# Kernel optimization log

Hardware: AMD Instinct MI355X
Metric: run time of the kernel (lower is better)

Reference implementation:

```python
import jax, jax.numpy as jnp
import numpy as np

B, V, N, IN_F, HEADS, OUT_F = 4, 4, 1000, 64, 4, 32
D = HEADS * OUT_F  # 128, concat=True
E = 64000
NEG_SLOPE = 0.2


def setup_inputs() -> dict:
    key = jax.random.key(0)
    ks = jax.random.split(key, 8)
    x = jax.random.normal(ks[0], (B, V, N, IN_F), jnp.float32)
    edge_index = jax.random.randint(ks[1], (2, E), 0, B * N, dtype=jnp.int64)
    W = jax.random.normal(ks[2], (HEADS * OUT_F, IN_F), jnp.float32) / np.sqrt(IN_F)
    att = jax.random.normal(ks[3], (1, HEADS, 2 * OUT_F), jnp.float32) * 0.1
    in_proj_w = jax.random.normal(ks[4], (3 * D, D), jnp.float32) / np.sqrt(D)
    in_proj_b = jnp.zeros((3 * D,), jnp.float32)
    out_proj_w = jax.random.normal(ks[5], (D, D), jnp.float32) / np.sqrt(D)
    out_proj_b = jnp.zeros((D,), jnp.float32)
    bias = jnp.zeros((D,), jnp.float32)
    return dict(x=x, W=W, att=att, in_proj_w=in_proj_w, in_proj_b=in_proj_b,
                out_proj_w=out_proj_w, out_proj_b=out_proj_b, bias=bias,
                edge_index=edge_index)


def reference(x, W, att, in_proj_w, in_proj_b, out_proj_w, out_proj_b, bias, edge_index):
    Bx, Vx, Nx, _ = x.shape
    Ntot = Bx * Nx
    # intra-view GAT: shared W across views
    h = jnp.einsum('bvni,oi->bvno', x, W).reshape(Bx, Vx, Nx, HEADS, OUT_F)
    # block-diagonal placement: h_full[b*V+v, b*N:(b+1)*N] = h[b,v]
    ib = jnp.arange(Bx)
    hf = jnp.zeros((Bx, Vx, Bx, Nx, HEADS, OUT_F), x.dtype).at[ib, :, ib].set(h)
    h_full = hf.reshape(Bx * Vx, Ntot, HEADS, OUT_F)
    # add self loops
    loops = jnp.arange(Ntot, dtype=edge_index.dtype)
    src = jnp.concatenate([edge_index[0], loops])
    dst = jnp.concatenate([edge_index[1], loops])
    # attention scores (faithful to source: flatten h_full over (B*V, Ntot) and
    # index with raw node ids, i.e. gathers from block 0 only)
    h_flat = h_full.reshape(Bx * Vx * Ntot, HEADS, OUT_F)
    h_cat = jnp.concatenate([h_flat[src], h_flat[dst]], axis=-1)  # [Etot, H, 2*OUT]
    att_in = jax.nn.leaky_relu(h_cat, NEG_SLOPE)
    scores = jnp.sum(att * att_in, axis=-1)  # [Etot, HEADS]
    # per-destination segment softmax
    seg_max = jax.ops.segment_max(scores, dst, num_segments=Ntot)
    seg_max = jax.lax.stop_gradient(jnp.where(jnp.isfinite(seg_max), seg_max, 0.0))
    ex = jnp.exp(scores - seg_max[dst])
    denom = jax.ops.segment_sum(ex, dst, num_segments=Ntot)
    alpha = ex / (denom[dst] + 1e-16)  # [Etot, HEADS]
    # scatter-add aggregation, broadcast over B*V rows
    msgs = h_full[:, src] * alpha[None, :, :, None]  # [B*V, Etot, H, OUT]
    out_full = jnp.zeros_like(h_full).at[:, dst].add(msgs)
    # extract each graph's own node block
    out = out_full.reshape(Bx, Vx, Bx, Nx, HEADS, OUT_F)[ib, :, ib]  # [B,V,N,H,OUT]
    h_gat = out.reshape(Bx, Vx, Nx, HEADS * OUT_F)  # concat heads
    # inter-view mixing: MHA over the V axis per node
    seq = h_gat.transpose(0, 2, 1, 3).reshape(Bx * Nx, Vx, D)
    q, k, v = jnp.split(seq @ in_proj_w.T + in_proj_b, 3, axis=-1)
    hd = D // HEADS
    sp = lambda t: t.reshape(Bx * Nx, Vx, HEADS, hd).transpose(0, 2, 1, 3)
    q, k, v = sp(q), sp(k), sp(v)
    aw = jax.nn.softmax(jnp.einsum('bhqd,bhkd->bhqk', q, k) / jnp.sqrt(jnp.asarray(hd, x.dtype)), axis=-1)
    ao = jnp.einsum('bhqk,bhkd->bhqd', aw, v).transpose(0, 2, 1, 3).reshape(Bx * Nx, Vx, D)
    mixed = ao @ out_proj_w.T + out_proj_b
    h_mixed = mixed.reshape(Bx, Nx, Vx, D).transpose(0, 2, 1, 3)  # [B,V,N,D]
    return h_mixed + bias
```

## Files before the change

kernel.cpp:

```cpp
#include <hip/hip_runtime.h>

#define NN 1000
#define HEADS_ 4
#define DM 128
#define EE 64000
#define NTOT 4000
#define ETOT 68000
#define CAP 48
#define EB 34

template <int K, int SCORE>
__device__ void gemm_tile(int mi, int ni,
                          const float* __restrict__ A, const float* __restrict__ Wt,
                          float* __restrict__ C, int N,
                          const float* __restrict__ att,
                          float* __restrict__ ssrc, float* __restrict__ sdst) {
  __shared__ float As[128 * 64];
  __shared__ float Bs[64 * 64];
  int tid = threadIdx.x;
  int m0 = mi * 128, n0 = ni * 64;
  int tx = tid & 15, ty = tid >> 4;
  const float4* A4 = (const float4*)A;
  const float4* W4 = (const float4*)Wt;
  float acc[8][4] = {};

  for (int c = 0; c < K / 64; ++c) {
    __syncthreads();
    {
      int q = tid & 15;
      int r0 = tid >> 4;
#pragma unroll
      for (int p = 0; p < 8; ++p) {
        int r = r0 + p * 16;
        float4 v = A4[(size_t)(m0 + r) * (K / 4) + c * 16 + q];
        *(float4*)&As[r * 64 + ((q ^ ((r >> 2) & 15)) << 2)] = v;
      }
#pragma unroll
      for (int p = 0; p < 4; ++p) {
        int r = r0 + p * 16;
        float4 v = W4[(size_t)(n0 + r) * (K / 4) + c * 16 + q];
        *(float4*)&Bs[r * 64 + ((q ^ ((r >> 2) & 15)) << 2)] = v;
      }
    }
    __syncthreads();
#pragma unroll 4
    for (int q = 0; q < 16; ++q) {
      float4 a[8], b[4];
#pragma unroll
      for (int i = 0; i < 8; ++i) {
        int r = ty * 8 + i;
        a[i] = *(const float4*)&As[r * 64 + ((q ^ ((r >> 2) & 15)) << 2)];
      }
#pragma unroll
      for (int j = 0; j < 4; ++j) {
        int rn = tx * 4 + j;
        b[j] = *(const float4*)&Bs[rn * 64 + ((q ^ ((rn >> 2) & 15)) << 2)];
      }
#pragma unroll
      for (int i = 0; i < 8; ++i)
#pragma unroll
        for (int j = 0; j < 4; ++j)
          acc[i][j] += a[i].x * b[j].x + a[i].y * b[j].y
                     + a[i].z * b[j].z + a[i].w * b[j].w;
    }
  }

  int nc = n0 + tx * 4;
#pragma unroll
  for (int i = 0; i < 8; ++i) {
    int m = m0 + ty * 8 + i;
    float4 o = make_float4(acc[i][0], acc[i][1], acc[i][2], acc[i][3]);
    *(float4*)&C[(size_t)m * N + nc] = o;
  }

  if (SCORE && m0 < NN) {
    int hsel = tx >> 3;
    int h = ni * 2 + hsel;
    int kb = (tx & 7) * 4;
    float a0[4], a1[4];
#pragma unroll
    for (int j = 0; j < 4; ++j) {
      a0[j] = att[h * 64 + kb + j];
      a1[j] = att[h * 64 + 32 + kb + j];
    }
#pragma unroll
    for (int i = 0; i < 8; ++i) {
      int m = m0 + ty * 8 + i;
      float p0 = 0.f, p1 = 0.f;
#pragma unroll
      for (int j = 0; j < 4; ++j) {
        float g = acc[i][j];
        float lr = g > 0.f ? g : 0.2f * g;
        p0 += a0[j] * lr;
        p1 += a1[j] * lr;
      }
      p0 += __shfl_xor(p0, 1, 16); p1 += __shfl_xor(p1, 1, 16);
      p0 += __shfl_xor(p0, 2, 16); p1 += __shfl_xor(p1, 2, 16);
      p0 += __shfl_xor(p0, 4, 16); p1 += __shfl_xor(p1, 4, 16);
      if ((tx & 7) == 0 && m < NN) {
        ssrc[m * HEADS_ + h] = p0;
        sdst[m * HEADS_ + h] = p1;
      }
    }
  }
}

__global__ __launch_bounds__(256) void k1_kernel(const float* __restrict__ x,
                                                 const float* __restrict__ W,
                                                 const float* __restrict__ att,
                                                 float* __restrict__ hbuf,
                                                 float* __restrict__ ssrc,
                                                 float* __restrict__ sdst,
                                                 const int* __restrict__ ei,
                                                 int* __restrict__ cnt,
                                                 int* __restrict__ elist) {
  int bid = blockIdx.x;
  if (bid < 250) {
    gemm_tile<64, 1>(bid >> 1, bid & 1, x, W, hbuf, 128, att, ssrc, sdst);
  } else {
    for (int e = (bid - 250) * 256 + threadIdx.x; e < ETOT; e += EB * 256) {
      int s, d;
      if (e < EE) { s = ei[e]; d = ei[EE + e]; }
      else { s = d = e - EE; }
      int pos = atomicAdd(&cnt[d], 1);
      if (pos < CAP) elist[d * CAP + pos] = s;
    }
  }
}

__global__ __launch_bounds__(256) void gather_kernel(const int* __restrict__ cnt,
                                                     const int* __restrict__ elist,
                                                     const float* __restrict__ ssrc,
                                                     const float* __restrict__ sdst,
                                                     const float* __restrict__ hbuf,
                                                     float* __restrict__ hgat) {
  __shared__ int   srcs[2][CAP];
  __shared__ float exs[2][CAP][HEADS_];
  int li = threadIdx.x >> 7;
  int t = threadIdx.x & 127;
  int d = blockIdx.x * 2 + li;
  int b = d / NN;
  int v = t >> 5, q = t & 31, h = q >> 3;
  int m = cnt[d]; if (m > CAP) m = CAP;
  for (int base = 0; base < m; base += 32) {
    int i = base + (t >> 2);
    if (i < m) {
      int s = elist[d * CAP + i];
      if ((t & 3) == 0) srcs[li][i] = s;
      float sc = ssrc[s * HEADS_ + (t & 3)] + sdst[d * HEADS_ + (t & 3)];
      exs[li][i][t & 3] = __expf(sc);
    }
  }
  __syncthreads();
  float den = 1e-16f;
  float4 acc = make_float4(0.f, 0.f, 0.f, 0.f);
  const float* hbase = hbuf + ((size_t)(b * 4 + v) * NN) * DM + q * 4;
  for (int i = 0; i < m; ++i) {
    float ex = exs[li][i][h];
    den += ex;
    unsigned sl = (unsigned)(srcs[li][i] - b * NN);
    if (sl < NN) {
      float4 hv = *(const float4*)(hbase + (size_t)sl * DM);
      acc.x += ex * hv.x; acc.y += ex * hv.y;
      acc.z += ex * hv.z; acc.w += ex * hv.w;
    }
  }
  float r = 1.f / den;
  acc.x *= r; acc.y *= r; acc.z *= r; acc.w *= r;
  *(float4*)&hgat[((size_t)(d * 4 + v)) * DM + q * 4] = acc;
}

#define QS 388

__global__ __launch_bounds__(512) void fused3_kernel(const float* __restrict__ hgat,
                                                     const float* __restrict__ inw,
                                                     const float* __restrict__ inb,
                                                     const float* __restrict__ outw,
                                                     const float* __restrict__ outb,
                                                     const float* __restrict__ bias,
                                                     float* __restrict__ out) {
  extern __shared__ float smem[];
  float* As = smem;
  float* Bs = smem + 4096;
  float* qk = smem + 12288;
  float* ao = qk;

  int tid = threadIdx.x;
  int g0 = blockIdx.x * 16;
  int tx = tid & 31, ty = tid >> 5;

  const float4* H4 = (const float4*)(hgat + (size_t)(g0 * 4) * DM);
  const float4* W4 = (const float4*)inw;

  float acc[3][4][4] = {};
#pragma unroll
  for (int c = 0; c < 2; ++c) {
#pragma unroll
    for (int ni = 0; ni < 3; ++ni) {
      __syncthreads();
      {
        int q = tid & 15, r0 = tid >> 4;
        if (ni == 0) {
#pragma unroll
          for (int p = 0; p < 2; ++p) {
            int r = r0 + p * 32;
            float4 v = H4[r * 32 + c * 16 + q];
            *(float4*)&As[r * 64 + ((q ^ ((r >> 2) & 15)) << 2)] = v;
          }
        }
#pragma unroll
        for (int p = 0; p < 4; ++p) {
          int r = r0 + p * 32;
          float4 v = W4[(size_t)(ni * 128 + r) * 32 + c * 16 + q];
          *(float4*)&Bs[r * 64 + ((q ^ ((r >> 2) & 15)) << 2)] = v;
        }
      }
      __syncthreads();
#pragma unroll 4
      for (int q = 0; q < 16; ++q) {
        float4 a[4], b[4];
        int sa = (q ^ ty) << 2;
        int sb = (q ^ (tx & 15)) << 2;
#pragma unroll
        for (int i = 0; i < 4; ++i)
          a[i] = *(const float4*)&As[(ty * 4 + i) * 64 + sa];
#pragma unroll
        for (int j = 0; j < 4; ++j)
          b[j] = *(const float4*)&Bs[(tx * 4 + j) * 64 + sb];
#pragma unroll
        for (int i = 0; i < 4; ++i)
#pragma unroll
          for (int j = 0; j < 4; ++j)
            acc[ni][i][j] += a[i].x * b[j].x + a[i].y * b[j].y
                           + a[i].z * b[j].z + a[i].w * b[j].w;
      }
    }
  }

#pragma unroll
  for (int ni = 0; ni < 3; ++ni) {
    int nc = ni * 128 + tx * 4;
    float4 bb = *(const float4*)&inb[nc];
#pragma unroll
    for (int i = 0; i < 4; ++i) {
      int r = ty * 4 + i;
      *(float4*)&qk[r * QS + nc] =
          make_float4(acc[ni][i][0] + bb.x, acc[ni][i][1] + bb.y,
                      acc[ni][i][2] + bb.z, acc[ni][i][3] + bb.w);
    }
  }
  __syncthreads();

  int ln = tid >> 5;
  int vq2 = (tid >> 3) & 3, h2 = (tid >> 1) & 3, s2 = tid & 1;
  float aww[4];
  {
    const float* qr = &qk[(ln * 4 + vq2) * QS + h2 * 32 + s2 * 16];
    float4 qv[4];
#pragma unroll
    for (int u = 0; u < 4; ++u) qv[u] = *(const float4*)&qr[u * 4];
    float sc[4];
#pragma unroll
    for (int vk = 0; vk < 4; ++vk) {
      const float* kr = &qk[(ln * 4 + vk) * QS + 128 + h2 * 32 + s2 * 16];
      float s = 0.f;
#pragma unroll
      for (int u = 0; u < 4; ++u) {
        float4 kv = *(const float4*)&kr[u * 4];
        s += qv[u].x * kv.x + qv[u].y * kv.y + qv[u].z * kv.z + qv[u].w * kv.w;
      }
      sc[vk] = s;
    }
#pragma unroll
    for (int vk = 0; vk < 4; ++vk)
      sc[vk] = (sc[vk] + __shfl_xor(sc[vk], 1)) * 0.17677669529663687f;
    float mx = fmaxf(fmaxf(sc[0], sc[1]), fmaxf(sc[2], sc[3]));
    float e0 = __expf(sc[0] - mx), e1 = __expf(sc[1] - mx);
    float e2 = __expf(sc[2] - mx), e3 = __expf(sc[3] - mx);
    float inv = 1.f / (e0 + e1 + e2 + e3);
    aww[0] = e0 * inv; aww[1] = e1 * inv; aww[2] = e2 * inv; aww[3] = e3 * inv;
  }

  float4 o[4];
#pragma unroll
  for (int u = 0; u < 4; ++u) o[u] = make_float4(0.f, 0.f, 0.f, 0.f);
#pragma unroll
  for (int vk = 0; vk < 4; ++vk) {
    const float* vr = &qk[(ln * 4 + vk) * QS + 256 + h2 * 32 + s2 * 16];
    float w = aww[vk];
#pragma unroll
    for (int u = 0; u < 4; ++u) {
      float4 vv = *(const float4*)&vr[u * 4];
      o[u].x += w * vv.x; o[u].y += w * vv.y;
      o[u].z += w * vv.z; o[u].w += w * vv.w;
    }
  }
  __syncthreads();
  {
    int r = ln * 4 + vq2;
#pragma unroll
    for (int u = 0; u < 4; ++u) {
      int qp = h2 * 8 + s2 * 4 + u;
      int cc = qp >> 4, qg = qp & 15;
      *(float4*)&ao[cc * 4096 + r * 64 + ((qg ^ (ln & 15)) << 2)] = o[u];
    }
  }
  __syncthreads();

  float oc[4][4] = {};
  const float4* O4 = (const float4*)outw;
#pragma unroll
  for (int c = 0; c < 2; ++c) {
    {
      int q = tid & 15, r0 = tid >> 4;
#pragma unroll
      for (int p = 0; p < 4; ++p) {
        int r = r0 + p * 32;
        float4 v = O4[(size_t)r * 32 + c * 16 + q];
        *(float4*)&Bs[r * 64 + ((q ^ ((r >> 2) & 15)) << 2)] = v;
      }
    }
    __syncthreads();
#pragma unroll 4
    for (int q = 0; q < 16; ++q) {
      float4 a[4], b[4];
      int sa = (q ^ ty) << 2;
      int sb = (q ^ (tx & 15)) << 2;
#pragma unroll
      for (int i = 0; i < 4; ++i)
        a[i] = *(const float4*)&ao[c * 4096 + (ty * 4 + i) * 64 + sa];
#pragma unroll
      for (int j = 0; j < 4; ++j)
        b[j] = *(const float4*)&Bs[(tx * 4 + j) * 64 + sb];
#pragma unroll
      for (int i = 0; i < 4; ++i)
#pragma unroll
        for (int j = 0; j < 4; ++j)
          oc[i][j] += a[i].x * b[j].x + a[i].y * b[j].y
                    + a[i].z * b[j].z + a[i].w * b[j].w;
    }
    __syncthreads();
  }

  {
    int nc = tx * 4;
    float4 ob = make_float4(outb[nc] + bias[nc], outb[nc + 1] + bias[nc + 1],
                            outb[nc + 2] + bias[nc + 2], outb[nc + 3] + bias[nc + 3]);
#pragma unroll
    for (int i = 0; i < 4; ++i) {
      int r = ty * 4 + i;
      int node = g0 + (r >> 2), v = r & 3;
      int bg = node / NN, n = node - bg * NN;
      int om = (bg * 4 + v) * NN + n;
      *(float4*)&out[(size_t)om * DM + nc] =
          make_float4(oc[i][0] + ob.x, oc[i][1] + ob.y,
                      oc[i][2] + ob.z, oc[i][3] + ob.w);
    }
  }
}

extern "C" void kernel_launch(void* const* d_in, const int* in_sizes, int n_in,
                              void* d_out, int out_size, void* d_ws, size_t ws_size,
                              hipStream_t stream) {
  const float* x    = (const float*)d_in[0];
  const float* W    = (const float*)d_in[1];
  const float* att  = (const float*)d_in[2];
  const float* inw  = (const float*)d_in[3];
  const float* inb  = (const float*)d_in[4];
  const float* outw = (const float*)d_in[5];
  const float* outb = (const float*)d_in[6];
  const float* bias = (const float*)d_in[7];
  const int*   ei   = (const int*)d_in[8];
  float* out = (float*)d_out;

  float* ws = (float*)d_ws;
  float* hbuf  = ws;
  float* hgat  = ws + 2100000;
  float* ssrc  = ws + 12500000;
  float* sdst  = ssrc + 16000;
  int*   cnt   = (int*)(sdst + 16000);
  int*   elist = cnt + 4000;

  static int lds_opt_in = 0;
  if (!lds_opt_in) {
    hipFuncSetAttribute((const void*)fused3_kernel,
                        hipFuncAttributeMaxDynamicSharedMemorySize, 160 * 1024);
    lds_opt_in = 1;
  }

  hipMemsetAsync(ssrc, 0, 36000 * sizeof(float), stream);

  k1_kernel<<<250 + EB, 256, 0, stream>>>(x, W, att, hbuf, ssrc, sdst, ei, cnt, elist);
  gather_kernel<<<NTOT / 2, 256, 0, stream>>>(cnt, elist, ssrc, sdst, hbuf, hgat);
  fused3_kernel<<<250, 512, 148480, stream>>>(hgat, inw, inb, outw, outb, bias, out);
}
```

Measured before the change: 144.4 us.

## Fuse GAT gather into MHA kernel and shrink first GEMM tile

The neighbour gather/softmax-aggregation stage is folded into the inter-view attention kernel. Each block now builds its 64 rows of aggregated features directly in shared memory instead of writing hgat to global memory and reading it back, which also removes one kernel launch. The first projection GEMM switches from 128x64 to 64x64 tiles, doubling its block count to 500 for better occupancy. The trade-off is that the gather now runs with only 250 blocks and a different thread mapping, giving it less parallelism for latency hiding.

```diff
diff --git a/kernel.cpp b/kernel.cpp
--- a/kernel.cpp
+++ b/kernel.cpp
@@ -8,56 +8,54 @@
 #define ETOT 68000
 #define CAP 48
 #define EB 34
-
-template <int K, int SCORE>
-__device__ void gemm_tile(int mi, int ni,
-                          const float* __restrict__ A, const float* __restrict__ Wt,
-                          float* __restrict__ C, int N,
-                          const float* __restrict__ att,
-                          float* __restrict__ ssrc, float* __restrict__ sdst) {
-  __shared__ float As[128 * 64];
+#define QS 388
+
+template <int KK, int SCORE>
+__device__ void gemm64(int mi, int ni,
+                       const float* __restrict__ A, const float* __restrict__ Wt,
+                       float* __restrict__ C, int N,
+                       const float* __restrict__ att,
+                       float* __restrict__ ssrc, float* __restrict__ sdst) {
+  __shared__ float As[64 * 64];
   __shared__ float Bs[64 * 64];
   int tid = threadIdx.x;
-  int m0 = mi * 128, n0 = ni * 64;
+  int m0 = mi * 64, n0 = ni * 64;
   int tx = tid & 15, ty = tid >> 4;
   const float4* A4 = (const float4*)A;
   const float4* W4 = (const float4*)Wt;
-  float acc[8][4] = {};
-
-  for (int c = 0; c < K / 64; ++c) {
+  float acc[4][4] = {};
+
+  for (int c = 0; c < KK / 64; ++c) {
     __syncthreads();
     {
-      int q = tid & 15;
-      int r0 = tid >> 4;
-#pragma unroll
-      for (int p = 0; p < 8; ++p) {
-        int r = r0 + p * 16;
-        float4 v = A4[(size_t)(m0 + r) * (K / 4) + c * 16 + q];
-        *(float4*)&As[r * 64 + ((q ^ ((r >> 2) & 15)) << 2)] = v;
-      }
+      int q = tid & 15, r0 = tid >> 4;
 #pragma unroll
       for (int p = 0; p < 4; ++p) {
         int r = r0 + p * 16;
-        float4 v = W4[(size_t)(n0 + r) * (K / 4) + c * 16 + q];
+        float4 v = A4[(size_t)(m0 + r) * (KK / 4) + c * 16 + q];
+        *(float4*)&As[r * 64 + ((q ^ ((r >> 2) & 15)) << 2)] = v;
+      }
+#pragma unroll
+      for (int p = 0; p < 4; ++p) {
+        int r = r0 + p * 16;
+        float4 v = W4[(size_t)(n0 + r) * (KK / 4) + c * 16 + q];
         *(float4*)&Bs[r * 64 + ((q ^ ((r >> 2) & 15)) << 2)] = v;
       }
     }
     __syncthreads();
 #pragma unroll 4
     for (int q = 0; q < 16; ++q) {
-      float4 a[8], b[4];
-#pragma unroll
-      for (int i = 0; i < 8; ++i) {
-        int r = ty * 8 + i;
-        a[i] = *(const float4*)&As[r * 64 + ((q ^ ((r >> 2) & 15)) << 2)];
-      }
-#pragma unroll
-      for (int j = 0; j < 4; ++j) {
-        int rn = tx * 4 + j;
-        b[j] = *(const float4*)&Bs[rn * 64 + ((q ^ ((rn >> 2) & 15)) << 2)];
-      }
-#pragma unroll
-      for (int i = 0; i < 8; ++i)
+      float4 a[4], b[4];
+      int sa = (q ^ ty) << 2;
+      int sb = (q ^ tx) << 2;
+#pragma unroll
+      for (int i = 0; i < 4; ++i)
+        a[i] = *(const float4*)&As[(ty * 4 + i) * 64 + sa];
+#pragma unroll
+      for (int j = 0; j < 4; ++j)
+        b[j] = *(const float4*)&Bs[(tx * 4 + j) * 64 + sb];
+#pragma unroll
+      for (int i = 0; i < 4; ++i)
 #pragma unroll
         for (int j = 0; j < 4; ++j)
           acc[i][j] += a[i].x * b[j].x + a[i].y * b[j].y
@@ -67,10 +65,10 @@
 
   int nc = n0 + tx * 4;
 #pragma unroll
-  for (int i = 0; i < 8; ++i) {
-    int m = m0 + ty * 8 + i;
-    float4 o = make_float4(acc[i][0], acc[i][1], acc[i][2], acc[i][3]);
-    *(float4*)&C[(size_t)m * N + nc] = o;
+  for (int i = 0; i < 4; ++i) {
+    int m = m0 + ty * 4 + i;
+    *(float4*)&C[(size_t)m * N + nc] =
+        make_float4(acc[i][0], acc[i][1], acc[i][2], acc[i][3]);
   }
 
   if (SCORE && m0 < NN) {
@@ -84,8 +82,8 @@
       a1[j] = att[h * 64 + 32 + kb + j];
     }
 #pragma unroll
-    for (int i = 0; i < 8; ++i) {
-      int m = m0 + ty * 8 + i;
+    for (int i = 0; i < 4; ++i) {
+      int m = m0 + ty * 4 + i;
       float p0 = 0.f, p1 = 0.f;
 #pragma unroll
       for (int j = 0; j < 4; ++j) {
@@ -115,10 +113,10 @@
                                                  int* __restrict__ cnt,
                                                  int* __restrict__ elist) {
   int bid = blockIdx.x;
-  if (bid < 250) {
-    gemm_tile<64, 1>(bid >> 1, bid & 1, x, W, hbuf, 128, att, ssrc, sdst);
+  if (bid < 500) {
+    gemm64<64, 1>(bid >> 1, bid & 1, x, W, hbuf, 128, att, ssrc, sdst);
   } else {
-    for (int e = (bid - 250) * 256 + threadIdx.x; e < ETOT; e += EB * 256) {
+    for (int e = (bid - 500) * 256 + threadIdx.x; e < ETOT; e += EB * 256) {
       int s, d;
       if (e < EE) { s = ei[e]; d = ei[EE + e]; }
       else { s = d = e - EE; }
@@ -128,114 +126,118 @@
   }
 }
 
-__global__ __launch_bounds__(256) void gather_kernel(const int* __restrict__ cnt,
-                                                     const int* __restrict__ elist,
-                                                     const float* __restrict__ ssrc,
-                                                     const float* __restrict__ sdst,
-                                                     const float* __restrict__ hbuf,
-                                                     float* __restrict__ hgat) {
-  __shared__ int   srcs[2][CAP];
-  __shared__ float exs[2][CAP][HEADS_];
-  int li = threadIdx.x >> 7;
-  int t = threadIdx.x & 127;
-  int d = blockIdx.x * 2 + li;
-  int b = d / NN;
-  int v = t >> 5, q = t & 31, h = q >> 3;
-  int m = cnt[d]; if (m > CAP) m = CAP;
-  for (int base = 0; base < m; base += 32) {
-    int i = base + (t >> 2);
-    if (i < m) {
-      int s = elist[d * CAP + i];
-      if ((t & 3) == 0) srcs[li][i] = s;
-      float sc = ssrc[s * HEADS_ + (t & 3)] + sdst[d * HEADS_ + (t & 3)];
-      exs[li][i][t & 3] = __expf(sc);
-    }
-  }
-  __syncthreads();
-  float den = 1e-16f;
-  float4 acc = make_float4(0.f, 0.f, 0.f, 0.f);
-  const float* hbase = hbuf + ((size_t)(b * 4 + v) * NN) * DM + q * 4;
-  for (int i = 0; i < m; ++i) {
-    float ex = exs[li][i][h];
-    den += ex;
-    unsigned sl = (unsigned)(srcs[li][i] - b * NN);
-    if (sl < NN) {
-      float4 hv = *(const float4*)(hbase + (size_t)sl * DM);
-      acc.x += ex * hv.x; acc.y += ex * hv.y;
-      acc.z += ex * hv.z; acc.w += ex * hv.w;
-    }
-  }
-  float r = 1.f / den;
-  acc.x *= r; acc.y *= r; acc.z *= r; acc.w *= r;
-  *(float4*)&hgat[((size_t)(d * 4 + v)) * DM + q * 4] = acc;
-}
-
-#define QS 388
-
-__global__ __launch_bounds__(512) void fused3_kernel(const float* __restrict__ hgat,
-                                                     const float* __restrict__ inw,
-                                                     const float* __restrict__ inb,
-                                                     const float* __restrict__ outw,
-                                                     const float* __restrict__ outb,
-                                                     const float* __restrict__ bias,
-                                                     float* __restrict__ out) {
+__global__ __launch_bounds__(512) void mega_kernel(const int* __restrict__ cnt,
+                                                   const int* __restrict__ elist,
+                                                   const float* __restrict__ ssrc,
+                                                   const float* __restrict__ sdst,
+                                                   const float* __restrict__ hbuf,
+                                                   const float* __restrict__ inw,
+                                                   const float* __restrict__ inb,
+                                                   const float* __restrict__ outw,
+                                                   const float* __restrict__ outb,
+                                                   const float* __restrict__ bias,
+                                                   float* __restrict__ out) {
   extern __shared__ float smem[];
-  float* As = smem;
-  float* Bs = smem + 4096;
-  float* qk = smem + 12288;
-  float* ao = qk;
+  float* As   = smem;
+  float* rg2  = smem + 8448;
+  float* exsF = rg2;
+  int*   srcsI = (int*)(rg2 + 3072);
+  float* Bs   = rg2 + 4096;
+  float* qk   = rg2;
+  float* ao   = rg2;
+  float* Bs2  = rg2 + 8192;
 
   int tid = threadIdx.x;
-  int g0 = blockIdx.x * 16;
+  int g0n = blockIdx.x * 16;
+
+  {
+    int ln = tid >> 5, t32 = tid & 31;
+    int d = g0n + ln;
+    int m = cnt[d]; if (m > CAP) m = CAP;
+    for (int base = 0; base < m; base += 8) {
+      int i = base + (t32 >> 2);
+      if (i < m) {
+        int s = elist[d * CAP + i];
+        if ((t32 & 3) == 0) srcsI[ln * CAP + i] = s;
+        float sc = ssrc[s * HEADS_ + (t32 & 3)] + sdst[d * HEADS_ + (t32 & 3)];
+        exsF[ln * 192 + i * 4 + (t32 & 3)] = __expf(sc);
+      }
+    }
+  }
+  __syncthreads();
+
+  {
+    int r = tid >> 3, g = tid & 7;
+    int ln = r >> 2, v = r & 3;
+    int d = g0n + ln, b = d / NN;
+    int m = cnt[d]; if (m > CAP) m = CAP;
+    const float* hbase = hbuf + ((size_t)(b * 4 + v) * NN) * DM + g * 4;
+    float4 a0 = make_float4(0.f, 0.f, 0.f, 0.f), a1 = a0, a2 = a0, a3 = a0;
+    float4 den = make_float4(1e-16f, 1e-16f, 1e-16f, 1e-16f);
+    for (int i = 0; i < m; ++i) {
+      float4 ex = *(const float4*)&exsF[ln * 192 + i * 4];
+      unsigned sl = (unsigned)(srcsI[ln * CAP + i] - b * NN);
+      unsigned sc = sl < NN ? sl : 0u;
+      const float* hrow = hbase + (size_t)sc * DM;
+      float4 h0 = *(const float4*)(hrow);
+      float4 h1 = *(const float4*)(hrow + 32);
+      float4 h2 = *(const float4*)(hrow + 64);
+      float4 h3 = *(const float4*)(hrow + 96);
+      den.x += ex.x; den.y += ex.y; den.z += ex.z; den.w += ex.w;
+      float w0 = sl < NN ? ex.x : 0.f, w1 = sl < NN ? ex.y : 0.f;
+      float w2 = sl < NN ? ex.z : 0.f, w3 = sl < NN ? ex.w : 0.f;
+      a0.x += w0 * h0.x; a0.y += w0 * h0.y; a0.z += w0 * h0.z; a0.w += w0 * h0.w;
+      a1.x += w1 * h1.x; a1.y += w1 * h1.y; a1.z += w1 * h1.z; a1.w += w1 * h1.w;
+      a2.x += w2 * h2.x; a2.y += w2 * h2.y; a2.z += w2 * h2.z; a2.w += w2 * h2.w;
+      a3.x += w3 * h3.x; a3.y += w3 * h3.y; a3.z += w3 * h3.z; a3.w += w3 * h3.w;
+    }
+    float i0 = 1.f / den.x, i1 = 1.f / den.y, i2 = 1.f / den.z, i3 = 1.f / den.w;
+    *(float4*)&As[r * 132 +       g * 4] = make_float4(a0.x * i0, a0.y * i0, a0.z * i0, a0.w * i0);
+    *(float4*)&As[r * 132 +  32 + g * 4] = make_float4(a1.x * i1, a1.y * i1, a1.z * i1, a1.w * i1);
+    *(float4*)&As[r * 132 +  64 + g * 4] = make_float4(a2.x * i2, a2.y * i2, a2.z * i2, a2.w * i2);
+    *(float4*)&As[r * 132 +  96 + g * 4] = make_float4(a3.x * i3, a3.y * i3, a3.z * i3, a3.w * i3);
+  }
+
   int tx = tid & 31, ty = tid >> 5;
-
-  const float4* H4 = (const float4*)(hgat + (size_t)(g0 * 4) * DM);
-  const float4* W4 = (const float4*)inw;
-
   float acc[3][4][4] = {};
-#pragma unroll
-  for (int c = 0; c < 2; ++c) {
-#pragma unroll
-    for (int ni = 0; ni < 3; ++ni) {
-      __syncthreads();
-      {
-        int q = tid & 15, r0 = tid >> 4;
-        if (ni == 0) {
-#pragma unroll
-          for (int p = 0; p < 2; ++p) {
+  {
+    const float4* W4 = (const float4*)inw;
+#pragma unroll
+    for (int c = 0; c < 2; ++c) {
+#pragma unroll
+      for (int ni = 0; ni < 3; ++ni) {
+        __syncthreads();
+        {
+          int q = tid & 15, r0 = tid >> 4;
+#pragma unroll
+          for (int p = 0; p < 4; ++p) {
             int r = r0 + p * 32;
-            float4 v = H4[r * 32 + c * 16 + q];
-            *(float4*)&As[r * 64 + ((q ^ ((r >> 2) & 15)) << 2)] = v;
+            float4 v = W4[(size_t)(ni * 128 + r) * 32 + c * 16 + q];
+            *(float4*)&Bs[r * 64 + ((q ^ ((r >> 2) & 15)) << 2)] = v;
           }
         }
-#pragma unroll
-        for (int p = 0; p < 4; ++p) {
-          int r = r0 + p * 32;
-          float4 v = W4[(size_t)(ni * 128 + r) * 32 + c * 16 + q];
-          *(float4*)&Bs[r * 64 + ((q ^ ((r >> 2) & 15)) << 2)] = v;
+        __syncthreads();
+#pragma unroll 4
+        for (int q = 0; q < 16; ++q) {
+          float4 a[4], b[4];
+          int sb = (q ^ (tx & 15)) << 2;
+#pragma unroll
+          for (int i = 0; i < 4; ++i)
+            a[i] = *(const float4*)&As[(ty * 4 + i) * 132 + c * 64 + q * 4];
+#pragma unroll
+          for (int j = 0; j < 4; ++j)
+            b[j] = *(const float4*)&Bs[(tx * 4 + j) * 64 + sb];
+#pragma unroll
+          for (int i = 0; i < 4; ++i)
+#pragma unroll
+            for (int j = 0; j < 4; ++j)
+              acc[ni][i][j] += a[i].x * b[j].x + a[i].y * b[j].y
+                             + a[i].z * b[j].z + a[i].w * b[j].w;
         }
       }
-      __syncthreads();
-#pragma unroll 4
-      for (int q = 0; q < 16; ++q) {
-        float4 a[4], b[4];
-        int sa = (q ^ ty) << 2;
-        int sb = (q ^ (tx & 15)) << 2;
-#pragma unroll
-        for (int i = 0; i < 4; ++i)
-          a[i] = *(const float4*)&As[(ty * 4 + i) * 64 + sa];
-#pragma unroll
-        for (int j = 0; j < 4; ++j)
-          b[j] = *(const float4*)&Bs[(tx * 4 + j) * 64 + sb];
-#pragma unroll
-        for (int i = 0; i < 4; ++i)
-#pragma unroll
-          for (int j = 0; j < 4; ++j)
-            acc[ni][i][j] += a[i].x * b[j].x + a[i].y * b[j].y
-                           + a[i].z * b[j].z + a[i].w * b[j].w;
-      }
-    }
-  }
+    }
+  }
+  __syncthreads();
 
 #pragma unroll
   for (int ni = 0; ni < 3; ++ni) {
@@ -317,13 +319,13 @@
       for (int p = 0; p < 4; ++p) {
         int r = r0 + p * 32;
         float4 v = O4[(size_t)r * 32 + c * 16 + q];
-        *(float4*)&Bs[r * 64 + ((q ^ ((r >> 2) & 15)) << 2)] = v;
+        *(float4*)&Bs2[r * 64 + ((q ^ ((r >> 2) & 15)) << 2)] = v;
       }
     }
     __syncthreads();
 #pragma unroll 4
     for (int q = 0; q < 16; ++q) {
-      float4 a[4], b[4];
+      float4 a[4], bq[4];
       int sa = (q ^ ty) << 2;
       int sb = (q ^ (tx & 15)) << 2;
 #pragma unroll
@@ -331,13 +333,13 @@
         a[i] = *(const float4*)&ao[c * 4096 + (ty * 4 + i) * 64 + sa];
 #pragma unroll
       for (int j = 0; j < 4; ++j)
-        b[j] = *(const float4*)&Bs[(tx * 4 + j) * 64 + sb];
+        bq[j] = *(const float4*)&Bs2[(tx * 4 + j) * 64 + sb];
 #pragma unroll
       for (int i = 0; i < 4; ++i)
 #pragma unroll
         for (int j = 0; j < 4; ++j)
-          oc[i][j] += a[i].x * b[j].x + a[i].y * b[j].y
-                    + a[i].z * b[j].z + a[i].w * b[j].w;
+          oc[i][j] += a[i].x * bq[j].x + a[i].y * bq[j].y
+                    + a[i].z * bq[j].z + a[i].w * bq[j].w;
     }
     __syncthreads();
   }
@@ -349,9 +351,9 @@
 #pragma unroll
     for (int i = 0; i < 4; ++i) {
       int r = ty * 4 + i;
-      int node = g0 + (r >> 2), v = r & 3;
+      int node = g0n + (r >> 2), vv = r & 3;
       int bg = node / NN, n = node - bg * NN;
-      int om = (bg * 4 + v) * NN + n;
+      int om = (bg * 4 + vv) * NN + n;
       *(float4*)&out[(size_t)om * DM + nc] =
           make_float4(oc[i][0] + ob.x, oc[i][1] + ob.y,
                       oc[i][2] + ob.z, oc[i][3] + ob.w);
@@ -375,7 +377,6 @@
 
   float* ws = (float*)d_ws;
   float* hbuf  = ws;
-  float* hgat  = ws + 2100000;
   float* ssrc  = ws + 12500000;
   float* sdst  = ssrc + 16000;
   int*   cnt   = (int*)(sdst + 16000);
@@ -383,14 +384,14 @@
 
   static int lds_opt_in = 0;
   if (!lds_opt_in) {
-    hipFuncSetAttribute((const void*)fused3_kernel,
+    hipFuncSetAttribute((const void*)mega_kernel,
                         hipFuncAttributeMaxDynamicSharedMemorySize, 160 * 1024);
     lds_opt_in = 1;
   }
 
   hipMemsetAsync(ssrc, 0, 36000 * sizeof(float), stream);
 
-  k1_kernel<<<250 + EB, 256, 0, stream>>>(x, W, att, hbuf, ssrc, sdst, ei, cnt, elist);
-  gather_kernel<<<NTOT / 2, 256, 0, stream>>>(cnt, elist, ssrc, sdst, hbuf, hgat);
-  fused3_kernel<<<250, 512, 148480, stream>>>(hgat, inw, inb, outw, outb, bias, out);
+  k1_kernel<<<500 + EB, 256, 0, stream>>>(x, W, att, hbuf, ssrc, sdst, ei, cnt, elist);
+  mega_kernel<<<250, 512, 133120, stream>>>(cnt, elist, ssrc, sdst, hbuf,
+                                            inw, inb, outw, outb, bias, out);
 }
```

Result: faster. 138.2 us (median of 2 runs) (-4.3%).
